# Kernel tuning notes

Measured on AMD Instinct MI355X. Metric: run time of the kernel, lower is better.

## Reference

```python
import jax, jax.numpy as jnp
import numpy as np

T = 4096          # total tokens across ragged segments
H = 4096          # hidden_size
I = 11008         # intermediate_size
R = 16            # lora_rank
A = 4             # number of adapters (segments)


def setup_inputs() -> dict:
    key = jax.random.key(0)
    ks = jax.random.split(key, 12)
    inp = {
        "x": jax.random.normal(ks[0], (T, H), jnp.float32),
        "gate_w": jax.random.normal(ks[1], (I, H), jnp.float32) * (1.0 / np.sqrt(H)),
        "up_w": jax.random.normal(ks[2], (I, H), jnp.float32) * (1.0 / np.sqrt(H)),
        "down_w": jax.random.normal(ks[3], (H, I), jnp.float32) * (1.0 / np.sqrt(I)),
        "gate_wa": jax.random.normal(ks[4], (A, H, R), jnp.float32) * 0.01,
        "gate_wb": jax.random.normal(ks[5], (A, R, I), jnp.float32) * 0.01,
        "up_wa": jax.random.normal(ks[6], (A, H, R), jnp.float32) * 0.01,
        "up_wb": jax.random.normal(ks[7], (A, R, I), jnp.float32) * 0.01,
        "down_wa": jax.random.normal(ks[8], (A, I, R), jnp.float32) * 0.01,
        "down_wb": jax.random.normal(ks[9], (A, R, H), jnp.float32) * 0.01,
        "seg_ids": jnp.sort(jax.random.randint(ks[10], (T,), 0, A, jnp.int32)),
    }
    return inp


def _add_lora(y, inp, wa, wb, mask):
    # Segment-batched low-rank GEMM (Punica/S-LoRA add_lora):
    # for token t in segment a:  y[t] += inp[t] @ wa[a] @ wb[a]
    # mask: [T, A] one-hot of token->adapter assignment.
    # [A, T, R]: project into rank space for every adapter (R tiny), mask out
    xa = jnp.einsum('th,ahr->tar', inp, wa) * mask[:, :, None]   # [T, A, R]
    a, r = wb.shape[0], wb.shape[1]
    # collapse (A, R) so the expansion is one GEMM, no [A, T, out] intermediate
    delta = xa.reshape(inp.shape[0], a * r) @ wb.reshape(a * r, wb.shape[2])
    return y + delta


def reference(x, gate_w, up_w, down_w, gate_wa, gate_wb, up_wa, up_wb,
              down_wa, down_wb, seg_ids):
    mask = (seg_ids[:, None] == jnp.arange(A, dtype=seg_ids.dtype)[None, :]
            ).astype(x.dtype)                                    # [T, A]
    gate = x @ gate_w.T                                          # [T, I]
    gate = _add_lora(gate, x, gate_wa, gate_wb, mask)
    gate = jax.nn.silu(gate)
    up = x @ up_w.T                                              # [T, I]
    up = _add_lora(up, x, up_wa, up_wb, mask)
    t = gate * up
    down = t @ down_w.T                                          # [T, H]
    down = _add_lora(down, t, down_wa, down_wb, mask)
    return down
```

## Files before the change

kernel.cpp:

```cpp
#include <hip/hip_runtime.h>

#define T_TOK 4096
#define HID   4096
#define IMD   11008

using f32x4  = __attribute__((ext_vector_type(4))) float;
using bf16x8 = __attribute__((ext_vector_type(8))) __bf16;
union FragCast { int4 i; bf16x8 b; };

__device__ __forceinline__ unsigned f2bf_bits(float f) {
  unsigned u = __float_as_uint(f);
  return (u + 0x7fffu + ((u >> 16) & 1u)) >> 16;
}
__device__ __forceinline__ float bf2f(short s) {
  return __uint_as_float(((unsigned)(unsigned short)s) << 16);
}
__device__ __forceinline__ int4 cvt8(const float4 f0, const float4 f1) {
  int4 r;
  r.x = f2bf_bits(f0.x) | (f2bf_bits(f0.y) << 16);
  r.y = f2bf_bits(f0.z) | (f2bf_bits(f0.w) << 16);
  r.z = f2bf_bits(f1.x) | (f2bf_bits(f1.y) << 16);
  r.w = f2bf_bits(f1.z) | (f2bf_bits(f1.w) << 16);
  return r;
}
__device__ __forceinline__ void gload16(const void* g, void* l) {
  __builtin_amdgcn_global_load_lds(
      (__attribute__((address_space(1))) void*)g,
      (__attribute__((address_space(3))) void*)l, 16, 0, 0);
}

__global__ void cvt_pad(const float* __restrict__ in, short* __restrict__ out,
                        int C8, long ldin, long ldout) {
  long r = blockIdx.x;
  const float4* s = (const float4*)(in + r * ldin);
  int4* d = (int4*)(out + r * ldout);
  for (int c = threadIdx.x; c < C8; c += blockDim.x)
    d[c] = cvt8(s[2 * c], s[2 * c + 1]);
}

__global__ void build_wbT_pad(const float* __restrict__ wb,
                              short* __restrict__ out, int N, long ldout,
                              long K) {
  int n = blockIdx.x * blockDim.x + threadIdx.x;
  int ar = blockIdx.y;
  if (n < N) out[(long)n * ldout + K + ar] = (short)f2bf_bits(wb[(long)ar * N + n]);
}

__global__ void tail_copy(const short* __restrict__ src, short* dst, long ld) {
  dst[(long)blockIdx.x * ld + threadIdx.x] = src[blockIdx.x * 64 + threadIdx.x];
}

template <int KD, int NOUT>
__global__ __launch_bounds__(256)
void lora_proj(const short* __restrict__ Abf, long ldA,
               const float* __restrict__ wa0, const float* __restrict__ wa1,
               const int* __restrict__ seg, short* out0, long ld0, short* out1,
               long ld1) {
  __shared__ __align__(16) short rowbuf[KD];
  __shared__ float part[NOUT][4][16];
  int t = blockIdx.x, tid = threadIdx.x;
  int a = seg[t];
  const int4* src = (const int4*)(Abf + (long)t * ldA);
  for (int c = tid; c < KD / 8; c += 256) ((int4*)rowbuf)[c] = src[c];
  __syncthreads();
  int w = tid >> 6, l = tid & 63;
  int r = l & 15, g = l >> 4;
  const int HW = KD / 4;
  float s0 = 0.f, s1 = 0.f;
  const float* p0 = wa0 + (long)a * KD * 16 + r;
  const float* p1 = (NOUT == 2) ? (wa1 + (long)a * KD * 16 + r) : nullptr;
  int h = w * HW + g;
  for (int k = 0; k < HW / 4; ++k, h += 4) {
    float xv = bf2f(rowbuf[h]);
    s0 = fmaf(xv, p0[(long)h * 16], s0);
    if (NOUT == 2) s1 = fmaf(xv, p1[(long)h * 16], s1);
  }
  s0 += __shfl_xor(s0, 16); s0 += __shfl_xor(s0, 32);
  if (NOUT == 2) { s1 += __shfl_xor(s1, 16); s1 += __shfl_xor(s1, 32); }
  if (l < 16) { part[0][w][r] = s0; if (NOUT == 2) part[1][w][r] = s1; }
  __syncthreads();
  if (tid < 64 * NOUT) {
    int m = tid >> 6, ar = tid & 63;
    float v = 0.f;
    if ((ar >> 4) == a) {
      int r2 = ar & 15;
      v = part[m][0][r2] + part[m][1][r2] + part[m][2][r2] + part[m][3][r2];
    }
    short b = (short)f2bf_bits(v);
    if (m == 0) out0[(long)t * ld0 + ar] = b;
    else        out1[(long)t * ld1 + ar] = b;
  }
}

template <int MODE>
__global__ __launch_bounds__(512, 2)
void gemm256(const short* __restrict__ A, const short* __restrict__ B,
             const short* gbuf, short* outB, float* outF, int nby, long ldK,
             int iters, long ldo) {
  extern __shared__ __align__(16) char smem[];

  int nwg = gridDim.x;
  int orig = blockIdx.x;
  int q = nwg >> 3, rr = nwg & 7;
  int xcd = orig & 7, loc = orig >> 3;
  int swz = (xcd < rr ? xcd * (q + 1) : rr * (q + 1) + (xcd - rr) * q) + loc;
  int by = swz % nby, bx = swz / nby;
  long row0 = (long)bx * 256, col0 = (long)by * 256;

  int tid = threadIdx.x;
  int l = tid & 63, wid = tid >> 6;
  int wr = wid >> 2, wc = wid & 3;
  int lrow = l & 15, lhi = l >> 4, md = lrow & 7;

  const short* aP[4]; const short* bP[4];
  int dst[4];
#pragma unroll
  for (int k = 0; k < 4; ++k) {
    int idx = tid + k * 512;
    int r = idx >> 3, c8 = idx & 7;
    aP[k] = A + (row0 + r) * ldK + (c8 ^ (r & 7)) * 8;
    bP[k] = B + (col0 + r) * ldK + (c8 ^ (r & 7)) * 8;
    dst[k] = idx * 16;
  }

  auto stageA_h = [&](int bi, int h) {
    char* d = smem + bi * 32768;
    gload16(aP[2 * h], d + dst[2 * h]);         aP[2 * h] += 64;
    gload16(aP[2 * h + 1], d + dst[2 * h + 1]); aP[2 * h + 1] += 64;
  };
  auto stageB_h = [&](int bi, int h) {
    char* d = smem + 98304 + bi * 32768;
    gload16(bP[2 * h], d + dst[2 * h]);         bP[2 * h] += 64;
    gload16(bP[2 * h + 1], d + dst[2 * h + 1]); bP[2 * h + 1] += 64;
  };

  f32x4 acc[8][4];
  f32x4 zr = {0.f, 0.f, 0.f, 0.f};
#pragma unroll
  for (int mi = 0; mi < 8; ++mi)
#pragma unroll
    for (int ni = 0; ni < 4; ++ni) acc[mi][ni] = zr;

  const int csel0 = (lhi ^ md) * 16;
  const int csel1 = ((4 + lhi) ^ md) * 16;

  stageA_h(0, 0); stageA_h(0, 1);
  stageB_h(0, 0); stageB_h(0, 1);
  stageA_h(1, 0); stageA_h(1, 1);
  asm volatile("s_waitcnt vmcnt(4)" ::: "memory");
  asm volatile("s_barrier" ::: "memory");

  int ca = 0;
  for (int t = 0; t < iters; ++t) {
    const char* Ab = smem + ca * 32768;
    const char* Bb = smem + 98304 + (t & 1) * 32768;
    int na2 = (ca >= 1) ? ca - 1 : 2;
    int nb1 = (t + 1) & 1;
    bf16x8 bF[4][2];

#pragma unroll
    for (int p = 0; p < 4; ++p) {
      if (p == 0) {
#pragma unroll
        for (int ni = 0; ni < 4; ++ni) {
          const char* base = Bb + (wc * 64 + ni * 16 + lrow) * 128;
          FragCast f0, f1;
          f0.i = *(const int4*)(base + csel0);
          f1.i = *(const int4*)(base + csel1);
          bF[ni][0] = f0.b; bF[ni][1] = f1.b;
        }
      }
      bf16x8 aF[2][2];
#pragma unroll
      for (int m2 = 0; m2 < 2; ++m2) {
        const char* base = Ab + (wr * 128 + p * 32 + m2 * 16 + lrow) * 128;
        FragCast f0, f1;
        f0.i = *(const int4*)(base + csel0);
        f1.i = *(const int4*)(base + csel1);
        aF[m2][0] = f0.b; aF[m2][1] = f1.b;
      }
      if (p == 0 && t + 1 < iters) stageB_h(nb1, 0);
      if (p == 1 && t + 1 < iters) stageB_h(nb1, 1);
      if (p == 2 && t + 2 < iters) stageA_h(na2, 0);
      if (p == 3) {
        if (t + 2 < iters) {
          stageA_h(na2, 1);
          asm volatile("s_waitcnt vmcnt(4)" ::: "memory");
        } else {
          asm volatile("s_waitcnt vmcnt(0)" ::: "memory");
        }
      }
      asm volatile("s_barrier" ::: "memory");
      __builtin_amdgcn_s_setprio(1);
#pragma unroll
      for (int k = 0; k < 2; ++k)
#pragma unroll
        for (int m2 = 0; m2 < 2; ++m2)
#pragma unroll
          for (int ni = 0; ni < 4; ++ni)
            acc[p * 2 + m2][ni] = __builtin_amdgcn_mfma_f32_16x16x32_bf16(
                aF[m2][k], bF[ni][k], acc[p * 2 + m2][ni], 0, 0, 0);
      __builtin_amdgcn_s_setprio(0);
      asm volatile("s_barrier" ::: "memory");
    }
    ca = (ca == 2) ? 0 : ca + 1;
  }

#pragma unroll
  for (int mi = 0; mi < 8; ++mi)
#pragma unroll
    for (int ni = 0; ni < 4; ++ni)
#pragma unroll
      for (int j = 0; j < 4; ++j) {
        long grow = row0 + wr * 128 + mi * 16 + lhi * 4 + j;
        long gcol = col0 + wc * 64 + ni * 16 + lrow;
        long idx = grow * ldo + gcol;
        float v = acc[mi][ni][j];
        if constexpr (MODE == 0) {
          outB[idx] = (short)f2bf_bits(v);
        } else if constexpr (MODE == 1) {
          float g = bf2f(gbuf[idx]);
          float t2 = g * (1.f / (1.f + __expf(-g))) * v;
          outB[idx] = (short)f2bf_bits(t2);
        } else {
          outF[idx] = v;
        }
      }
}

extern "C" void kernel_launch(void* const* d_in, const int* in_sizes, int n_in,
                              void* d_out, int out_size, void* d_ws,
                              size_t ws_size, hipStream_t stream) {
  const float* x       = (const float*)d_in[0];
  const float* gate_w  = (const float*)d_in[1];
  const float* up_w    = (const float*)d_in[2];
  const float* down_w  = (const float*)d_in[3];
  const float* gate_wa = (const float*)d_in[4];
  const float* gate_wb = (const float*)d_in[5];
  const float* up_wa   = (const float*)d_in[6];
  const float* up_wb   = (const float*)d_in[7];
  const float* down_wa = (const float*)d_in[8];
  const float* down_wb = (const float*)d_in[9];
  const int*   seg     = (const int*)d_in[10];

  char* ws = (char*)d_ws;
  short* xg_pad = (short*)(ws);
  short* wA     = (short*)(ws + 34078720);
  short* wB     = (short*)(ws + 125665280);
  short* t_pad  = (short*)(ws + 217251840);
  short* xa_u   = (short*)(ws + 307953664);

  const int LDS_BYTES = 163840;
  hipFuncSetAttribute(reinterpret_cast<const void*>(&gemm256<0>),
                      hipFuncAttributeMaxDynamicSharedMemorySize, LDS_BYTES);
  hipFuncSetAttribute(reinterpret_cast<const void*>(&gemm256<1>),
                      hipFuncAttributeMaxDynamicSharedMemorySize, LDS_BYTES);
  hipFuncSetAttribute(reinterpret_cast<const void*>(&gemm256<2>),
                      hipFuncAttributeMaxDynamicSharedMemorySize, LDS_BYTES);

  cvt_pad<<<T_TOK, 256, 0, stream>>>(x, xg_pad, 512, HID, 4160);
  cvt_pad<<<IMD, 256, 0, stream>>>(gate_w, wA, 512, HID, 4160);
  cvt_pad<<<IMD, 256, 0, stream>>>(up_w, wB, 512, HID, 4160);
  build_wbT_pad<<<dim3(43, 64), 256, 0, stream>>>(gate_wb, wA, IMD, 4160, HID);
  build_wbT_pad<<<dim3(43, 64), 256, 0, stream>>>(up_wb, wB, IMD, 4160, HID);
  lora_proj<HID, 2><<<T_TOK, 256, 0, stream>>>(
      xg_pad, 4160, gate_wa, up_wa, seg, xg_pad + HID, 4160, xa_u, 64);

  gemm256<0><<<16 * 43, 512, LDS_BYTES, stream>>>(
      xg_pad, wA, nullptr, t_pad, nullptr, 43, 4160, 65, 11072);
  tail_copy<<<T_TOK, 64, 0, stream>>>(xa_u, xg_pad + HID, 4160);
  gemm256<1><<<16 * 43, 512, LDS_BYTES, stream>>>(
      xg_pad, wB, t_pad, t_pad, nullptr, 43, 4160, 65, 11072);

  cvt_pad<<<T_TOK, 256, 0, stream>>>(down_w, wA, 1376, IMD, 11072);
  build_wbT_pad<<<dim3(16, 64), 256, 0, stream>>>(down_wb, wA, HID, 11072, IMD);
  lora_proj<IMD, 1><<<T_TOK, 256, 0, stream>>>(
      t_pad, 11072, down_wa, nullptr, seg, t_pad + IMD, 11072, nullptr, 64);

  gemm256<2><<<16 * 16, 512, LDS_BYTES, stream>>>(
      t_pad, wA, nullptr, nullptr, (float*)d_out, 16, 11072, 173, 4096);
}
```

Before: 1.679 ms.

## Software-pipeline LDS fragment reads and use one barrier per K-iteration

Measured after the change: 1.867 ms. 11.2% more time.

```diff
diff --git a/kernel.cpp b/kernel.cpp
--- a/kernel.cpp
+++ b/kernel.cpp
@@ -113,25 +113,24 @@
   int lrow = l & 15, lhi = l >> 4, md = lrow & 7;
 
   const short* aP[4]; const short* bP[4];
-  int dst[4];
 #pragma unroll
   for (int k = 0; k < 4; ++k) {
     int idx = tid + k * 512;
     int r = idx >> 3, c8 = idx & 7;
     aP[k] = A + (row0 + r) * ldK + (c8 ^ (r & 7)) * 8;
     bP[k] = B + (col0 + r) * ldK + (c8 ^ (r & 7)) * 8;
-    dst[k] = idx * 16;
-  }
+  }
+  char* dbase = smem + tid * 16;
 
   auto stageA_h = [&](int bi, int h) {
-    char* d = smem + bi * 32768;
-    gload16(aP[2 * h], d + dst[2 * h]);         aP[2 * h] += 64;
-    gload16(aP[2 * h + 1], d + dst[2 * h + 1]); aP[2 * h + 1] += 64;
+    char* d = dbase + bi * 32768;
+    gload16(aP[2 * h], d + (2 * h) * 8192);         aP[2 * h] += 64;
+    gload16(aP[2 * h + 1], d + (2 * h + 1) * 8192); aP[2 * h + 1] += 64;
   };
   auto stageB_h = [&](int bi, int h) {
-    char* d = smem + 98304 + bi * 32768;
-    gload16(bP[2 * h], d + dst[2 * h]);         bP[2 * h] += 64;
-    gload16(bP[2 * h + 1], d + dst[2 * h + 1]); bP[2 * h + 1] += 64;
+    char* d = dbase + 98304 + bi * 32768;
+    gload16(bP[2 * h], d + (2 * h) * 8192);         bP[2 * h] += 64;
+    gload16(bP[2 * h + 1], d + (2 * h + 1) * 8192); bP[2 * h + 1] += 64;
   };
 
   f32x4 acc[8][4];
@@ -143,67 +142,75 @@
 
   const int csel0 = (lhi ^ md) * 16;
   const int csel1 = ((4 + lhi) ^ md) * 16;
+
+  bf16x8 bF[4][2], aF01[2][2], aF23[2][2], aF45[2][2], aF67[2][2];
+
+  auto readA = [&](const char* Ab, int mseg, bf16x8 (&aF)[2][2]) {
+#pragma unroll
+    for (int m2 = 0; m2 < 2; ++m2) {
+      const char* base = Ab + (wr * 128 + mseg * 32 + m2 * 16 + lrow) * 128;
+      FragCast f0, f1;
+      f0.i = *(const int4*)(base + csel0);
+      f1.i = *(const int4*)(base + csel1);
+      aF[m2][0] = f0.b; aF[m2][1] = f1.b;
+    }
+  };
+  auto readB = [&](const char* Bb) {
+#pragma unroll
+    for (int ni = 0; ni < 4; ++ni) {
+      const char* base = Bb + (wc * 64 + ni * 16 + lrow) * 128;
+      FragCast f0, f1;
+      f0.i = *(const int4*)(base + csel0);
+      f1.i = *(const int4*)(base + csel1);
+      bF[ni][0] = f0.b; bF[ni][1] = f1.b;
+    }
+  };
+  auto cluster = [&](int p, bf16x8 (&aF)[2][2]) {
+    __builtin_amdgcn_s_setprio(1);
+#pragma unroll
+    for (int k = 0; k < 2; ++k)
+#pragma unroll
+      for (int m2 = 0; m2 < 2; ++m2)
+#pragma unroll
+        for (int ni = 0; ni < 4; ++ni)
+          acc[p * 2 + m2][ni] = __builtin_amdgcn_mfma_f32_16x16x32_bf16(
+              aF[m2][k], bF[ni][k], acc[p * 2 + m2][ni], 0, 0, 0);
+    __builtin_amdgcn_s_setprio(0);
+  };
 
   stageA_h(0, 0); stageA_h(0, 1);
   stageB_h(0, 0); stageB_h(0, 1);
   stageA_h(1, 0); stageA_h(1, 1);
   asm volatile("s_waitcnt vmcnt(4)" ::: "memory");
-  asm volatile("s_barrier" ::: "memory");
+  __builtin_amdgcn_s_barrier();
+  readB(smem + 98304);
+  readA(smem, 0, aF01);
 
   int ca = 0;
+#pragma unroll 1
   for (int t = 0; t < iters; ++t) {
     const char* Ab = smem + ca * 32768;
-    const char* Bb = smem + 98304 + (t & 1) * 32768;
     int na2 = (ca >= 1) ? ca - 1 : 2;
     int nb1 = (t + 1) & 1;
-    bf16x8 bF[4][2];
-
-#pragma unroll
-    for (int p = 0; p < 4; ++p) {
-      if (p == 0) {
-#pragma unroll
-        for (int ni = 0; ni < 4; ++ni) {
-          const char* base = Bb + (wc * 64 + ni * 16 + lrow) * 128;
-          FragCast f0, f1;
-          f0.i = *(const int4*)(base + csel0);
-          f1.i = *(const int4*)(base + csel1);
-          bF[ni][0] = f0.b; bF[ni][1] = f1.b;
-        }
-      }
-      bf16x8 aF[2][2];
-#pragma unroll
-      for (int m2 = 0; m2 < 2; ++m2) {
-        const char* base = Ab + (wr * 128 + p * 32 + m2 * 16 + lrow) * 128;
-        FragCast f0, f1;
-        f0.i = *(const int4*)(base + csel0);
-        f1.i = *(const int4*)(base + csel1);
-        aF[m2][0] = f0.b; aF[m2][1] = f1.b;
-      }
-      if (p == 0 && t + 1 < iters) stageB_h(nb1, 0);
-      if (p == 1 && t + 1 < iters) stageB_h(nb1, 1);
-      if (p == 2 && t + 2 < iters) stageA_h(na2, 0);
-      if (p == 3) {
-        if (t + 2 < iters) {
-          stageA_h(na2, 1);
-          asm volatile("s_waitcnt vmcnt(4)" ::: "memory");
-        } else {
-          asm volatile("s_waitcnt vmcnt(0)" ::: "memory");
-        }
-      }
-      asm volatile("s_barrier" ::: "memory");
-      __builtin_amdgcn_s_setprio(1);
-#pragma unroll
-      for (int k = 0; k < 2; ++k)
-#pragma unroll
-        for (int m2 = 0; m2 < 2; ++m2)
-#pragma unroll
-          for (int ni = 0; ni < 4; ++ni)
-            acc[p * 2 + m2][ni] = __builtin_amdgcn_mfma_f32_16x16x32_bf16(
-                aF[m2][k], bF[ni][k], acc[p * 2 + m2][ni], 0, 0, 0);
-      __builtin_amdgcn_s_setprio(0);
-      asm volatile("s_barrier" ::: "memory");
-    }
-    ca = (ca == 2) ? 0 : ca + 1;
+    if (t + 1 < iters) stageB_h(nb1, 0);
+    readA(Ab, 1, aF23);
+    cluster(0, aF01);
+    if (t + 1 < iters) stageB_h(nb1, 1);
+    readA(Ab, 2, aF45);
+    cluster(1, aF23);
+    if (t + 2 < iters) stageA_h(na2, 0);
+    readA(Ab, 3, aF67);
+    cluster(2, aF45);
+    if (t + 2 < iters) stageA_h(na2, 1);
+    cluster(3, aF67);
+    if (t + 2 < iters)      asm volatile("s_waitcnt vmcnt(4)" ::: "memory");
+    else if (t + 1 < iters) asm volatile("s_waitcnt vmcnt(0)" ::: "memory");
+    if (t + 1 < iters) {
+      __builtin_amdgcn_s_barrier();
+      readB(smem + 98304 + nb1 * 32768);
+      readA(smem + ((ca < 2) ? ca + 1 : 0) * 32768, 0, aF01);
+    }
+    ca = (ca < 2) ? ca + 1 : 0;
   }
 
 #pragma unroll
```

## Make gate/up GEMMs persistent with XCD-local tile ownership and cross-tile prefetch

Applied to the files above, without the earlier changes.

After: 1.650 ms. No clear change (-1.7%).

```diff
diff --git a/kernel.cpp b/kernel.cpp
--- a/kernel.cpp
+++ b/kernel.cpp
@@ -30,12 +30,12 @@
 }
 
 __global__ void cvt_pad(const float* __restrict__ in, short* __restrict__ out,
-                        int C8, long ldin, long ldout) {
+                        int C8, int CT, long ldin, long ldout) {
   long r = blockIdx.x;
   const float4* s = (const float4*)(in + r * ldin);
   int4* d = (int4*)(out + r * ldout);
-  for (int c = threadIdx.x; c < C8; c += blockDim.x)
-    d[c] = cvt8(s[2 * c], s[2 * c + 1]);
+  for (int c = threadIdx.x; c < CT; c += blockDim.x)
+    d[c] = (c < C8) ? cvt8(s[2 * c], s[2 * c + 1]) : int4{0, 0, 0, 0};
 }
 
 __global__ void build_wbT_pad(const float* __restrict__ wb,
@@ -44,10 +44,6 @@
   int n = blockIdx.x * blockDim.x + threadIdx.x;
   int ar = blockIdx.y;
   if (n < N) out[(long)n * ldout + K + ar] = (short)f2bf_bits(wb[(long)ar * N + n]);
-}
-
-__global__ void tail_copy(const short* __restrict__ src, short* dst, long ld) {
-  dst[(long)blockIdx.x * ld + threadIdx.x] = src[blockIdx.x * 64 + threadIdx.x];
 }
 
 template <int KD, int NOUT>
@@ -94,9 +90,151 @@
 
 template <int MODE>
 __global__ __launch_bounds__(512, 2)
-void gemm256(const short* __restrict__ A, const short* __restrict__ B,
-             const short* gbuf, short* outB, float* outF, int nby, long ldK,
-             int iters, long ldo) {
+void gemm_gu(const short* __restrict__ A, const short* __restrict__ B,
+             const short* __restrict__ gbuf, short* __restrict__ outB,
+             int tilesPerXcd, long ldK, int iters, long ldo) {
+  extern __shared__ __align__(16) char smem[];
+
+  int xcd = blockIdx.x & 7, loc = blockIdx.x >> 3;
+  int tid = threadIdx.x;
+  int l = tid & 63, wid = tid >> 6;
+  int wr = wid >> 2, wc = wid & 3;
+  int lrow = l & 15, lhi = l >> 4, md = lrow & 7;
+  const int rr0 = tid >> 3;
+  const long cOff = (long)(((tid & 7) ^ (rr0 & 7)) * 8);
+
+  const int csel0 = (lhi ^ md) * 16;
+  const int csel1 = ((4 + lhi) ^ md) * 16;
+
+  const short* pA; const short* pB; long row0, col0;
+  auto setTile = [&](int idxInXcd) {
+    int gt = xcd * tilesPerXcd + idxInXcd;
+    row0 = (long)(gt & 15) * 256;
+    col0 = (long)(gt >> 4) * 256;
+    pA = A + (row0 + rr0) * ldK + cOff;
+    pB = B + (col0 + rr0) * ldK + cOff;
+  };
+  auto stA = [&](int bi, int h, int kt) {
+    char* d = smem + bi * 32768 + tid * 16;
+    const short* s = pA + (long)kt * 64 + (long)(2 * h) * 64 * ldK;
+    gload16(s, d + (2 * h) * 8192);
+    gload16(s + (long)64 * ldK, d + (2 * h + 1) * 8192);
+  };
+  auto stB = [&](int bi, int h, int kt) {
+    char* d = smem + 98304 + bi * 32768 + tid * 16;
+    const short* s = pB + (long)kt * 64 + (long)(2 * h) * 64 * ldK;
+    gload16(s, d + (2 * h) * 8192);
+    gload16(s + (long)64 * ldK, d + (2 * h + 1) * 8192);
+  };
+  auto prologue = [&]() {
+    stA(0, 0, 0); stA(0, 1, 0);
+    stB(0, 0, 0); stB(0, 1, 0);
+    stA(1, 0, 1); stA(1, 1, 1);
+  };
+
+  f32x4 zr = {0.f, 0.f, 0.f, 0.f};
+
+  int r = loc;
+  setTile(r);
+  prologue();
+
+  while (true) {
+    f32x4 acc[8][4];
+#pragma unroll
+    for (int mi = 0; mi < 8; ++mi)
+#pragma unroll
+      for (int ni = 0; ni < 4; ++ni) acc[mi][ni] = zr;
+
+    asm volatile("s_waitcnt vmcnt(4)" ::: "memory");
+    asm volatile("s_barrier" ::: "memory");
+
+    int ca = 0;
+#pragma unroll 1
+    for (int t = 0; t < iters; ++t) {
+      const char* Ab = smem + ca * 32768;
+      const char* Bb = smem + 98304 + (t & 1) * 32768;
+      int na2 = (ca >= 1) ? ca - 1 : 2;
+      int nb1 = (t + 1) & 1;
+      bf16x8 bF[4][2];
+
+#pragma unroll
+      for (int p = 0; p < 4; ++p) {
+        if (p == 0) {
+#pragma unroll
+          for (int ni = 0; ni < 4; ++ni) {
+            const char* base = Bb + (wc * 64 + ni * 16 + lrow) * 128;
+            FragCast f0, f1;
+            f0.i = *(const int4*)(base + csel0);
+            f1.i = *(const int4*)(base + csel1);
+            bF[ni][0] = f0.b; bF[ni][1] = f1.b;
+          }
+        }
+        bf16x8 aF[2][2];
+#pragma unroll
+        for (int m2 = 0; m2 < 2; ++m2) {
+          const char* base = Ab + (wr * 128 + p * 32 + m2 * 16 + lrow) * 128;
+          FragCast f0, f1;
+          f0.i = *(const int4*)(base + csel0);
+          f1.i = *(const int4*)(base + csel1);
+          aF[m2][0] = f0.b; aF[m2][1] = f1.b;
+        }
+        if (p == 0 && t + 1 < iters) stB(nb1, 0, t + 1);
+        if (p == 1 && t + 1 < iters) stB(nb1, 1, t + 1);
+        if (p == 2 && t + 2 < iters) stA(na2, 0, t + 2);
+        if (p == 3) {
+          if (t + 2 < iters) {
+            stA(na2, 1, t + 2);
+            asm volatile("s_waitcnt vmcnt(4)" ::: "memory");
+          } else {
+            asm volatile("s_waitcnt vmcnt(0)" ::: "memory");
+          }
+        }
+        asm volatile("s_barrier" ::: "memory");
+        __builtin_amdgcn_s_setprio(1);
+#pragma unroll
+        for (int k = 0; k < 2; ++k)
+#pragma unroll
+          for (int m2 = 0; m2 < 2; ++m2)
+#pragma unroll
+            for (int ni = 0; ni < 4; ++ni)
+              acc[p * 2 + m2][ni] = __builtin_amdgcn_mfma_f32_16x16x32_bf16(
+                  aF[m2][k], bF[ni][k], acc[p * 2 + m2][ni], 0, 0, 0);
+        __builtin_amdgcn_s_setprio(0);
+        asm volatile("s_barrier" ::: "memory");
+      }
+      ca = (ca == 2) ? 0 : ca + 1;
+    }
+
+    long crow = row0, ccol = col0;
+    r += 32;
+    bool hasNext = (r < tilesPerXcd);
+    if (hasNext) { setTile(r); prologue(); }
+
+#pragma unroll
+    for (int mi = 0; mi < 8; ++mi)
+#pragma unroll
+      for (int ni = 0; ni < 4; ++ni)
+#pragma unroll
+        for (int j = 0; j < 4; ++j) {
+          long grow = crow + wr * 128 + mi * 16 + lhi * 4 + j;
+          long gcol = ccol + wc * 64 + ni * 16 + lrow;
+          long idx = grow * ldo + gcol;
+          float v = acc[mi][ni][j];
+          if constexpr (MODE == 0) {
+            outB[idx] = (short)f2bf_bits(v);
+          } else {
+            float g = bf2f(gbuf[idx]);
+            float t2 = g * (1.f / (1.f + __expf(-g))) * v;
+            outB[idx] = (short)f2bf_bits(t2);
+          }
+        }
+    if (!hasNext) break;
+  }
+}
+
+__global__ __launch_bounds__(512, 2)
+void gemm_down(const short* __restrict__ A, const short* __restrict__ B,
+               float* outF, int nby, long ldK, int iters, long ldo) {
   extern __shared__ __align__(16) char smem[];
 
   int nwg = gridDim.x;
@@ -151,6 +289,7 @@
   asm volatile("s_barrier" ::: "memory");
 
   int ca = 0;
+#pragma unroll 1
   for (int t = 0; t < iters; ++t) {
     const char* Ab = smem + ca * 32768;
     const char* Bb = smem + 98304 + (t & 1) * 32768;
@@ -214,17 +353,7 @@
       for (int j = 0; j < 4; ++j) {
         long grow = row0 + wr * 128 + mi * 16 + lhi * 4 + j;
         long gcol = col0 + wc * 64 + ni * 16 + lrow;
-        long idx = grow * ldo + gcol;
-        float v = acc[mi][ni][j];
-        if constexpr (MODE == 0) {
-          outB[idx] = (short)f2bf_bits(v);
-        } else if constexpr (MODE == 1) {
-          float g = bf2f(gbuf[idx]);
-          float t2 = g * (1.f / (1.f + __expf(-g))) * v;
-          outB[idx] = (short)f2bf_bits(t2);
-        } else {
-          outF[idx] = v;
-        }
+        outF[grow * ldo + gcol] = acc[mi][ni][j];
       }
 }
 
@@ -245,38 +374,38 @@
 
   char* ws = (char*)d_ws;
   short* xg_pad = (short*)(ws);
-  short* wA     = (short*)(ws + 34078720);
-  short* wB     = (short*)(ws + 125665280);
-  short* t_pad  = (short*)(ws + 217251840);
-  short* xa_u   = (short*)(ws + 307953664);
-
-  const int LDS_BYTES = 163840;
-  hipFuncSetAttribute(reinterpret_cast<const void*>(&gemm256<0>),
-                      hipFuncAttributeMaxDynamicSharedMemorySize, LDS_BYTES);
-  hipFuncSetAttribute(reinterpret_cast<const void*>(&gemm256<1>),
-                      hipFuncAttributeMaxDynamicSharedMemorySize, LDS_BYTES);
-  hipFuncSetAttribute(reinterpret_cast<const void*>(&gemm256<2>),
-                      hipFuncAttributeMaxDynamicSharedMemorySize, LDS_BYTES);
-
-  cvt_pad<<<T_TOK, 256, 0, stream>>>(x, xg_pad, 512, HID, 4160);
-  cvt_pad<<<IMD, 256, 0, stream>>>(gate_w, wA, 512, HID, 4160);
-  cvt_pad<<<IMD, 256, 0, stream>>>(up_w, wB, 512, HID, 4160);
-  build_wbT_pad<<<dim3(43, 64), 256, 0, stream>>>(gate_wb, wA, IMD, 4160, HID);
-  build_wbT_pad<<<dim3(43, 64), 256, 0, stream>>>(up_wb, wB, IMD, 4160, HID);
+  short* wA     = (short*)(ws + 34603008);
+  short* wB     = (short*)(ws + 127598592);
+  short* t_pad  = (short*)(ws + 220594176);
+
+  const int LDS_G = 163840;
+  hipFuncSetAttribute(reinterpret_cast<const void*>(&gemm_gu<0>),
+                      hipFuncAttributeMaxDynamicSharedMemorySize, LDS_G);
+  hipFuncSetAttribute(reinterpret_cast<const void*>(&gemm_gu<1>),
+                      hipFuncAttributeMaxDynamicSharedMemorySize, LDS_G);
+  hipFuncSetAttribute(reinterpret_cast<const void*>(&gemm_down),
+                      hipFuncAttributeMaxDynamicSharedMemorySize, LDS_G);
+
+  cvt_pad<<<T_TOK, 256, 0, stream>>>(x, xg_pad, 512, 512, HID, 4224);
+  cvt_pad<<<IMD, 256, 0, stream>>>(gate_w, wA, 512, 528, HID, 4224);
+  cvt_pad<<<IMD, 256, 0, stream>>>(up_w, wB, 512, 528, HID, 4224);
+  build_wbT_pad<<<dim3(43, 64), 256, 0, stream>>>(gate_wb, wA, IMD, 4224, 4096);
+  build_wbT_pad<<<dim3(43, 64), 256, 0, stream>>>(up_wb, wB, IMD, 4224, 4160);
   lora_proj<HID, 2><<<T_TOK, 256, 0, stream>>>(
-      xg_pad, 4160, gate_wa, up_wa, seg, xg_pad + HID, 4160, xa_u, 64);
-
-  gemm256<0><<<16 * 43, 512, LDS_BYTES, stream>>>(
-      xg_pad, wA, nullptr, t_pad, nullptr, 43, 4160, 65, 11072);
-  tail_copy<<<T_TOK, 64, 0, stream>>>(xa_u, xg_pad + HID, 4160);
-  gemm256<1><<<16 * 43, 512, LDS_BYTES, stream>>>(
-      xg_pad, wB, t_pad, t_pad, nullptr, 43, 4160, 65, 11072);
-
-  cvt_pad<<<T_TOK, 256, 0, stream>>>(down_w, wA, 1376, IMD, 11072);
-  build_wbT_pad<<<dim3(16, 64), 256, 0, stream>>>(down_wb, wA, HID, 11072, IMD);
+      xg_pad, 4224, gate_wa, up_wa, seg, xg_pad + 4096, 4224, xg_pad + 4160,
+      4224);
+
+  gemm_gu<0><<<256, 512, LDS_G, stream>>>(xg_pad, wA, nullptr, t_pad,
+                                          86, 4224, 66, 11072);
+  gemm_gu<1><<<256, 512, LDS_G, stream>>>(xg_pad, wB, t_pad, t_pad,
+                                          86, 4224, 66, 11072);
+
+  cvt_pad<<<T_TOK, 256, 0, stream>>>(down_w, wA, 1376, 1376, IMD, 11072);
+  build_wbT_pad<<<dim3(16, 64), 256, 0, stream>>>(down_wb, wA, HID, 11072,
+                                                  IMD);
   lora_proj<IMD, 1><<<T_TOK, 256, 0, stream>>>(
       t_pad, 11072, down_wa, nullptr, seg, t_pad + IMD, 11072, nullptr, 64);
 
-  gemm256<2><<<16 * 16, 512, LDS_BYTES, stream>>>(
-      t_pad, wA, nullptr, nullptr, (float*)d_out, 16, 11072, 173, 4096);
-}
+  gemm_down<<<16 * 16, 512, LDS_G, stream>>>(t_pad, wA, (float*)d_out, 16,
+                                             11072, 173, 4096);
+}
```
